# Optimization experiments

Measured on AMD Instinct MI355X. Metric: run time of the kernel, lower is better.

Reference implementation:

```python
import jax, jax.numpy as jnp
import numpy as np

B_, H_, N_, L_ = 4, 512, 64, 2048  # batch, d_model, d_state/2 (conj pairs), seq len


def setup_inputs() -> dict:
    key = jax.random.key(0)
    ks = jax.random.split(key, 8)
    x = jax.random.normal(ks[0], (B_, H_, L_), jnp.float32)
    ln_w = jnp.ones((H_,), jnp.float32)
    ln_b = jnp.zeros((H_,), jnp.float32)
    # S4D-style init: dt log-uniform in [1e-3, 1e-1], A = -1/2 + i*pi*n (S4D-Lin)
    log_dt = jax.random.uniform(ks[1], (H_,), jnp.float32) * (np.log(0.1) - np.log(0.001)) + np.log(0.001)
    log_A_real = jnp.broadcast_to(jnp.log(jnp.float32(0.5)), (H_, N_))
    A_imag = jnp.broadcast_to(np.pi * jnp.arange(N_, dtype=np.float32), (H_, N_))
    B_re = jnp.ones((H_, N_), jnp.float32)
    B_im = jnp.zeros((H_, N_), jnp.float32)
    # 2 kernel channels for bidirectional
    C_re = jax.random.normal(ks[2], (2, H_, N_), jnp.float32) * (0.5 ** 0.5)
    C_im = jax.random.normal(ks[3], (2, H_, N_), jnp.float32) * (0.5 ** 0.5)
    D = jax.random.normal(ks[4], (H_,), jnp.float32)
    W_out = jax.random.normal(ks[5], (H_, H_), jnp.float32) / np.sqrt(H_)
    b_out = jnp.zeros((H_,), jnp.float32)
    return dict(x=x, ln_w=ln_w, ln_b=ln_b, log_dt=log_dt, log_A_real=log_A_real,
                A_imag=A_imag, B_re=B_re, B_im=B_im, C_re=C_re, C_im=C_im,
                D=D, W_out=W_out, b_out=b_out)


def _s4_layer(x, ln_w, ln_b, log_dt, log_A_real, A_imag, B_re, B_im, C_re, C_im, D, W_out, b_out):
    Bb, H, L = x.shape
    # ---- pre-norm LayerNorm over channel dim (module transposes to (B,L,H)) ----
    zt = x.transpose(0, 2, 1)                          # (B, L, H)
    mu = zt.mean(-1, keepdims=True)
    var = jnp.mean((zt - mu) ** 2, -1, keepdims=True)
    zt = (zt - mu) * jax.lax.rsqrt(var + 1e-5) * ln_w + ln_b
    z = zt.transpose(0, 2, 1)                          # (B, H, L)
    # ---- S4 diagonal SSM kernel, ZOH discretization, 2 channels (bidirectional) ----
    dt = jnp.exp(log_dt)[:, None]                      # (H, 1)
    A = -jnp.exp(log_A_real) + 1j * A_imag             # (H, N)
    dtA = A * dt                                       # (H, N)
    dB = (B_re + 1j * B_im) * (jnp.exp(dtA) - 1.0) / A # (H, N) discretized B
    CB = (C_re + 1j * C_im) * dB                       # (2, H, N)
    V = jnp.exp(dtA[:, :, None] * jnp.arange(L))       # (H, N, L) Vandermonde exp(l*dt*A)
    k = 2.0 * jnp.real(jnp.einsum('chn,hnl->chl', CB, V))  # (2, H, L)
    # ---- bidirectional: causal + flipped anticausal kernel, length 2L ----
    zpad = jnp.zeros_like(k[0])
    kb = jnp.concatenate([k[0], zpad], -1) + jnp.concatenate([zpad, k[1][:, ::-1]], -1)  # (H, 2L)
    # ---- FFT convolution ----
    k_f = jnp.fft.rfft(kb, n=2 * L)                    # (H, L+1)
    u_f = jnp.fft.rfft(z, n=2 * L)                     # (B, H, L+1)
    y = jnp.fft.irfft(u_f * k_f, n=2 * L)[..., :L]     # (B, H, L)
    y = y + z * D[:, None]                             # skip connection D*u
    y = jax.nn.gelu(y)                                 # default S4 activation
    y = jnp.einsum('oh,bhl->bol', W_out, y) + b_out[:, None]  # output linear (Conv1d k=1)
    return y + x                                       # residual of S4Layer


def reference(x, ln_w, ln_b, log_dt, log_A_real, A_imag, B_re, B_im, C_re, C_im, D, W_out, b_out):
    return _s4_layer(x, ln_w, ln_b, log_dt, log_A_real, A_imag, B_re, B_im, C_re, C_im, D, W_out, b_out)
```

## Files before the change

kernel.cpp:

```cpp
#include <hip/hip_runtime.h>
#include <math.h>

#define Bq 4
#define Hq 512
#define Nq 64
#define Lq 2048
#define PARAM (Hq*Nq)

__global__ __launch_bounds__(256)
void setup_kernel(const float* __restrict__ log_dt,
                  const float* __restrict__ log_A_real,
                  const float* __restrict__ A_imag,
                  const float* __restrict__ B_re, const float* __restrict__ B_im,
                  const float* __restrict__ C_re, const float* __restrict__ C_im,
                  float* __restrict__ a0, float* __restrict__ b0,
                  float* __restrict__ a1, float* __restrict__ b1,
                  float* __restrict__ pw, float* __restrict__ pwT,
                  const float* __restrict__ x, const float* __restrict__ lnw,
                  const float* __restrict__ lnb, float* __restrict__ z) {
    __shared__ float rs_[16][17], r2_[16][17], mu_s[16], sg_s[16];
    int bx = blockIdx.x;
    if (bx < 128) {
        int idx = bx * 256 + threadIdx.x;
        int h = idx >> 6, n = idx & 63;
        float dt = expf(log_dt[h]);
        float Ar = -expf(log_A_real[idx]);
        float Ai = A_imag[idx];
        float er = expf(Ar * dt);
        float wr = er * cosf(Ai * dt);
        float wi = er * sinf(Ai * dt);
        float mr = wr - 1.0f, mi = wi;
        float den = Ar * Ar + Ai * Ai;
        float qr = (mr * Ar + mi * Ai) / den;
        float qi = (mi * Ar - mr * Ai) / den;
        float Br = B_re[idx], Bi = B_im[idx];
        float dBr = Br * qr - Bi * qi;
        float dBi = Br * qi + Bi * qr;
        float cr = C_re[idx], ci = C_im[idx];
        a0[idx] =  2.0f * (cr * dBr - ci * dBi);
        b0[idx] = -2.0f * (cr * dBi + ci * dBr);
        cr = C_re[PARAM + idx]; ci = C_im[PARAM + idx];
        a1[idx] =  2.0f * (cr * dBr - ci * dBi);
        b1[idx] = -2.0f * (cr * dBi + ci * dBr);
        float c = 1.f, s = 0.f;
        float* base  = pw  + (size_t)h * 65 * 128 + 2 * n;
        float* baseT = pwT + (size_t)(h * 64 + n) * 132;
        for (int d = 0; d <= 64; ++d) {
            *(float2*)(base + (size_t)d * 128) = float2{c, s};
            *(float2*)(baseT + 2 * d)          = float2{c, s};
            float nc = c * wr - s * wi;
            float ns = c * wi + s * wr;
            c = nc; s = ns;
        }
        return;
    }
    int blk = bx - 128;
    int b  = blk / (Lq / 16);
    int l0 = (blk % (Lq / 16)) * 16;
    int tx = threadIdx.x & 15;
    int ty = threadIdx.x >> 4;
    const float* xb = x + (size_t)b * Hq * Lq;
    float s = 0.f, s2 = 0.f;
    for (int h = ty; h < Hq; h += 16) {
        float v = xb[h * Lq + l0 + tx];
        s += v; s2 += v * v;
    }
    rs_[ty][tx] = s; r2_[ty][tx] = s2;
    __syncthreads();
    if (ty == 0) {
        float a = 0.f, c = 0.f;
        #pragma unroll
        for (int i = 0; i < 16; ++i) { a += rs_[i][tx]; c += r2_[i][tx]; }
        float mu = a * (1.0f / Hq);
        float var = c * (1.0f / Hq) - mu * mu;
        mu_s[tx] = mu;
        sg_s[tx] = rsqrtf(var + 1e-5f);
    }
    __syncthreads();
    float mu = mu_s[tx], rs = sg_s[tx];
    float* zb = z + (size_t)b * Hq * Lq;
    for (int h = ty; h < Hq; h += 16) {
        float v = xb[h * Lq + l0 + tx];
        zb[h * Lq + l0 + tx] = (v - mu) * rs * lnw[h] + lnb[h];
    }
}

__global__ __launch_bounds__(256, 4)
void ssm_kernel(const float* __restrict__ z, const float* __restrict__ pw,
                const float* __restrict__ pwT,
                const float* __restrict__ a0, const float* __restrict__ b0,
                const float* __restrict__ a1, const float* __restrict__ b1,
                const float* __restrict__ Dv, float* __restrict__ u) {
    __shared__ float Zs[64][68];
    __shared__ float As[64][68];
    __shared__ float ks0[64], ks1[64], as0_[64], bs0_[64], as1_[64], bs1_[64];
    int h = blockIdx.x, bp = blockIdx.y;
    int t = threadIdx.x;
    int tx = t & 15, ty = t >> 4;
    const float* pwh  = pw  + (size_t)h * 65 * 128;
    const float* pwTh = pwT + (size_t)h * 64 * 132;
    {
        int cc = t & 31, rb = (t >> 5) & 1, jg = t >> 6;
        const float* zb = z + ((size_t)(2 * bp + rb) * Hq + h) * Lq;
        #pragma unroll
        for (int f = 0; f < 4; ++f) {
            float4 v = *(const float4*)(zb + cc * 64 + 16 * jg + 4 * f);
            Zs[16*jg+4*f+0][rb*32+cc] = v.x;
            Zs[16*jg+4*f+1][rb*32+cc] = v.y;
            Zs[16*jg+4*f+2][rb*32+cc] = v.z;
            Zs[16*jg+4*f+3][rb*32+cc] = v.w;
        }
    }
    if (t < 64) {
        as0_[t] = a0[h*64+t]; bs0_[t] = b0[h*64+t];
        as1_[t] = a1[h*64+t]; bs1_[t] = b1[h*64+t];
    }
    __syncthreads();
    if (t < 128) {
        int dir_ = t >> 6, d = t & 63;
        float acc2 = 0.f;
        if (dir_ == 0) {
            for (int n = 0; n < 64; ++n) {
                float2 v = *(const float2*)(pwTh + (size_t)n*132 + 2*d);
                acc2 = fmaf(as0_[n], v.x, acc2);
                acc2 = fmaf(bs0_[n], v.y, acc2);
            }
            ks0[d] = acc2;
        } else {
            for (int n = 0; n < 64; ++n) {
                float2 v = *(const float2*)(pwTh + (size_t)n*132 + 2*d);
                acc2 = fmaf(as1_[n], v.x, acc2);
                acc2 = fmaf(bs1_[n], v.y, acc2);
            }
            ks1[d] = acc2;
        }
    }
    float d0R[4][4] = {}, d0I[4][4] = {}, d1R[4][4] = {}, d1I[4][4] = {};
    #pragma unroll 2
    for (int k = 0; k < 64; ++k) {
        const float4* pr = (const float4*)(pwh + (size_t)k*128 + 8*tx);
        float4 p0 = pr[0], p1 = pr[1];
        float c4[4] = {p0.x, p0.z, p1.x, p1.z};
        float s4[4] = {p0.y, p0.w, p1.y, p1.w};
        float4 zf = *(const float4*)&Zs[63-k][4*ty];
        float4 zg = *(const float4*)&Zs[k][4*ty];
        #pragma unroll
        for (int rr = 0; rr < 4; ++rr) {
            #pragma unroll
            for (int q = 0; q < 4; ++q) {
                float zq0 = (&zf.x)[q], zq1 = (&zg.x)[q];
                d0R[rr][q] = fmaf(c4[rr], zq0, d0R[rr][q]);
                d0I[rr][q] = fmaf(s4[rr], zq0, d0I[rr][q]);
                d1R[rr][q] = fmaf(c4[rr], zq1, d1R[rr][q]);
                d1I[rr][q] = fmaf(s4[rr], zq1, d1I[rr][q]);
            }
        }
    }
    const float4* pr64 = (const float4*)(pwh + (size_t)64*128 + 8*tx);
    float4 w0v = pr64[0], w1v = pr64[1];
    float wc[4] = {w0v.x, w0v.z, w1v.x, w1v.z};
    float wn[4] = {w0v.y, w0v.w, w1v.y, w1v.w};
    int bS = ty >> 3, g = ty & 7;
    float* Vs = &As[0][0];
    #pragma unroll
    for (int rr = 0; rr < 4; ++rr) {
        float vr = 0.f, vi = 0.f;
        #pragma unroll
        for (int q = 0; q < 4; ++q) {
            float nr = fmaf(wc[rr], vr, fmaf(-wn[rr], vi, d0R[rr][q]));
            float ni = fmaf(wn[rr], vr, fmaf(wc[rr], vi, d0I[rr][q]));
            vr = nr; vi = ni;
        }
        *(float2*)(Vs + (size_t)((bS)*8+g)*130 + 2*(4*tx+rr)) = float2{vr, vi};
        vr = 0.f; vi = 0.f;
        #pragma unroll
        for (int q = 3; q >= 0; --q) {
            float nr = fmaf(wc[rr], vr, fmaf(-wn[rr], vi, d1R[rr][q]));
            float ni = fmaf(wn[rr], vr, fmaf(wc[rr], vi, d1I[rr][q]));
            vr = nr; vi = ni;
        }
        *(float2*)(Vs + (size_t)((2+bS)*8+g)*130 + 2*(4*tx+rr)) = float2{vr, vi};
    }
    __syncthreads();
    {
        int dir_ = t >> 7, bS_ = (t >> 6) & 1, n_ = t & 63;
        float2 wv = *(const float2*)(pwh + (size_t)64*128 + 2*n_);
        float w2r = fmaf(wv.x, wv.x, -(wv.y*wv.y));
        float w2i = 2.f*wv.x*wv.y;
        float Tr = fmaf(w2r, w2r, -(w2i*w2i));
        float Ti = 2.f*w2r*w2i;
        float* row = Vs + (size_t)(dir_*2+bS_)*8*130 + 2*n_;
        float er = 0.f, ei = 0.f;
        #pragma unroll
        for (int s2 = 0; s2 < 8; ++s2) {
            int g2 = dir_ ? (7 - s2) : s2;
            float* p2 = row + g2*130;
            float vr2 = p2[0], vi2 = p2[1];
            p2[0] = er; p2[1] = ei;
            float nr = fmaf(Tr, er, fmaf(-Ti, ei, vr2));
            float ni = fmaf(Ti, er, fmaf(Tr, ei, vi2));
            er = nr; ei = ni;
        }
    }
    __syncthreads();
    #pragma unroll
    for (int rr = 0; rr < 4; ++rr) {
        float2 E0 = *(const float2*)(Vs + (size_t)((bS)*8+g)*130 + 2*(4*tx+rr));
        float trr = E0.x, tii = E0.y;
        #pragma unroll
        for (int q = 0; q < 4; ++q) {
            float dr = d0R[rr][q], di = d0I[rr][q];
            d0R[rr][q] = trr; d0I[rr][q] = tii;
            float nr = fmaf(wc[rr], trr, fmaf(-wn[rr], tii, dr));
            float ni = fmaf(wn[rr], trr, fmaf(wc[rr], tii, di));
            trr = nr; tii = ni;
        }
        float2 E1 = *(const float2*)(Vs + (size_t)((2+bS)*8+g)*130 + 2*(4*tx+rr));
        trr = E1.x; tii = E1.y;
        #pragma unroll
        for (int q = 3; q >= 0; --q) {
            float dr = d1R[rr][q], di = d1I[rr][q];
            d1R[rr][q] = trr; d1I[rr][q] = tii;
            float nr = fmaf(wc[rr], trr, fmaf(-wn[rr], tii, dr));
            float ni = fmaf(wn[rr], trr, fmaf(wc[rr], tii, di));
            trr = nr; tii = ni;
        }
    }
    __syncthreads();
    int si = t & 63, kg = t >> 6;
    float2 pv[8];
    float acc[4][4] = {};
    for (int p = 0; p < 5; ++p) {
        if (p == 0) {
            #pragma unroll
            for (int q = 0; q < 16; ++q) {
                int kk = 16*kg + q;
                int d = si - kk;
                As[kk][si] = (d >= 0) ? ks0[d] : ks1[-d-1];
            }
        } else {
            const float* as_ = (p < 3) ? as0_ : as1_;
            const float* bs_ = (p < 3) ? bs0_ : bs1_;
            #pragma unroll
            for (int q = 0; q < 16; ++q) {
                int j = q >> 1;
                int n = 32*((p < 3) ? (p-1) : (p-3)) + 8*kg + j;
                float vx = pv[j].x, vy = pv[j].y;
                As[16*kg+q][si] = ((q&1) == 0) ? fmaf(as_[n], vx, bs_[n]*vy)
                                               : fmaf(bs_[n], vx, -as_[n]*vy);
            }
            if (p == 1 && tx < 8) {
                #pragma unroll
                for (int rr = 0; rr < 4; ++rr) {
                    int ml = 8*tx + 2*rr;
                    float4 vR; vR.x = d0R[rr][0]; vR.y = d0R[rr][1];
                    vR.z = d0R[rr][2]; vR.w = d0R[rr][3];
                    float4 vI; vI.x = d0I[rr][0]; vI.y = d0I[rr][1];
                    vI.z = d0I[rr][2]; vI.w = d0I[rr][3];
                    *(float4*)&Zs[ml][4*ty]   = vR;
                    *(float4*)&Zs[ml+1][4*ty] = vI;
                }
            } else if (p == 2 && tx >= 8) {
                #pragma unroll
                for (int rr = 0; rr < 4; ++rr) {
                    int ml = 8*(tx-8) + 2*rr;
                    float4 vR; vR.x = d0R[rr][0]; vR.y = d0R[rr][1];
                    vR.z = d0R[rr][2]; vR.w = d0R[rr][3];
                    float4 vI; vI.x = d0I[rr][0]; vI.y = d0I[rr][1];
                    vI.z = d0I[rr][2]; vI.w = d0I[rr][3];
                    *(float4*)&Zs[ml][4*ty]   = vR;
                    *(float4*)&Zs[ml+1][4*ty] = vI;
                }
            } else if (p == 3 && tx < 8) {
                #pragma unroll
                for (int rr = 0; rr < 4; ++rr) {
                    int ml = 8*tx + 2*rr;
                    float4 vR; vR.x = d1R[rr][0]; vR.y = d1R[rr][1];
                    vR.z = d1R[rr][2]; vR.w = d1R[rr][3];
                    float4 vI; vI.x = d1I[rr][0]; vI.y = d1I[rr][1];
                    vI.z = d1I[rr][2]; vI.w = d1I[rr][3];
                    *(float4*)&Zs[ml][4*ty]   = vR;
                    *(float4*)&Zs[ml+1][4*ty] = vI;
                }
            } else if (p == 4 && tx >= 8) {
                #pragma unroll
                for (int rr = 0; rr < 4; ++rr) {
                    int ml = 8*(tx-8) + 2*rr;
                    float4 vR; vR.x = d1R[rr][0]; vR.y = d1R[rr][1];
                    vR.z = d1R[rr][2]; vR.w = d1R[rr][3];
                    float4 vI; vI.x = d1I[rr][0]; vI.y = d1I[rr][1];
                    vI.z = d1I[rr][2]; vI.w = d1I[rr][3];
                    *(float4*)&Zs[ml][4*ty]   = vR;
                    *(float4*)&Zs[ml+1][4*ty] = vI;
                }
            }
        }
        __syncthreads();
        if (p < 4) {
            int pn = p + 1;
            int pp = (pn < 3) ? (pn-1) : (pn-3);
            int dsel = (pn < 3) ? (si + 1) : (63 - si);
            #pragma unroll
            for (int j2 = 0; j2 < 8; ++j2) {
                int n = 32*pp + 8*kg + j2;
                pv[j2] = *(const float2*)(pwTh + (size_t)n*132 + 2*dsel);
            }
        }
        #pragma unroll 8
        for (int kk = 0; kk < 64; ++kk) {
            float4 av = *(const float4*)&As[kk][4*tx];
            float4 bv = *(const float4*)&Zs[kk][4*ty];
            #pragma unroll
            for (int ii = 0; ii < 4; ++ii) {
                float a = (&av.x)[ii];
                acc[ii][0] = fmaf(a, bv.x, acc[ii][0]);
                acc[ii][1] = fmaf(a, bv.y, acc[ii][1]);
                acc[ii][2] = fmaf(a, bv.z, acc[ii][2]);
                acc[ii][3] = fmaf(a, bv.w, acc[ii][3]);
            }
        }
        __syncthreads();
    }
    float dv = Dv[h];
    #pragma unroll
    for (int q = 0; q < 4; ++q) {
        int cc2 = 4*ty + q;
        int b2 = 2*bp + (cc2 >> 5), ch2 = cc2 & 31;
        size_t base = ((size_t)b2 * Hq + h) * Lq + ch2 * 64 + 4 * tx;
        float4 zr = *(const float4*)(z + base);
        float vv[4];
        vv[0] = acc[0][q] + dv * zr.x;
        vv[1] = acc[1][q] + dv * zr.y;
        vv[2] = acc[2][q] + dv * zr.z;
        vv[3] = acc[3][q] + dv * zr.w;
        #pragma unroll
        for (int i = 0; i < 4; ++i) {
            float v = vv[i];
            float tt = tanhf(0.7978845608028654f * (v + 0.044715f * v * v * v));
            vv[i] = 0.5f * v * (1.0f + tt);
        }
        float4 r; r.x = vv[0]; r.y = vv[1]; r.z = vv[2]; r.w = vv[3];
        *(float4*)(u + base) = r;
    }
}

__global__ __launch_bounds__(512, 4)
void gemm_kernel(const float* __restrict__ u, const float* __restrict__ W,
                 const float* __restrict__ bias, const float* __restrict__ x,
                 float* __restrict__ out) {
    int l0 = blockIdx.x * 64;
    int o0 = blockIdx.y * 128;
    int b  = blockIdx.z;
    int tid = threadIdx.x;
    __shared__ float Ws[2][32][132];
    __shared__ float Us[2][32][68];
    const float* ub = u + (size_t)b * Hq * Lq;
    float acc[4][4] = {};
    int wo = tid >> 4, wl = tid & 15;
    int sj = tid & 31, so = tid >> 5;
    int sl = tid & 63, sk = tid >> 6;
    float wreg[8], ureg[4];
    #pragma unroll
    for (int r = 0; r < 8; ++r) wreg[r] = W[(size_t)(o0 + so + 16*r) * Hq + sj];
    #pragma unroll
    for (int r = 0; r < 4; ++r) ureg[r] = ub[(size_t)(4*sk + r) * Lq + l0 + sl];
    #pragma unroll
    for (int r = 0; r < 8; ++r) Ws[0][sj][so + 16*r] = wreg[r];
    #pragma unroll
    for (int r = 0; r < 4; ++r) Us[0][4*sk + r][sl] = ureg[r];
    __syncthreads();
    for (int t = 0; t < Hq / 32; ++t) {
        int cur = t & 1;
        if (t < 15) {
            int k0 = (t + 1) * 32;
            #pragma unroll
            for (int r = 0; r < 8; ++r)
                wreg[r] = W[(size_t)(o0 + so + 16*r) * Hq + k0 + sj];
            #pragma unroll
            for (int r = 0; r < 4; ++r)
                ureg[r] = ub[(size_t)(k0 + 4*sk + r) * Lq + l0 + sl];
        }
        #pragma unroll 8
        for (int j = 0; j < 32; ++j) {
            float4 av = *(const float4*)&Ws[cur][j][4 * wo];
            float4 bv = *(const float4*)&Us[cur][j][4 * wl];
            #pragma unroll
            for (int io = 0; io < 4; ++io) {
                float a = (&av.x)[io];
                acc[io][0] = fmaf(a, bv.x, acc[io][0]);
                acc[io][1] = fmaf(a, bv.y, acc[io][1]);
                acc[io][2] = fmaf(a, bv.z, acc[io][2]);
                acc[io][3] = fmaf(a, bv.w, acc[io][3]);
            }
        }
        if (t < 15) {
            int nxt = cur ^ 1;
            #pragma unroll
            for (int r = 0; r < 8; ++r) Ws[nxt][sj][so + 16*r] = wreg[r];
            #pragma unroll
            for (int r = 0; r < 4; ++r) Us[nxt][4*sk + r][sl] = ureg[r];
        }
        __syncthreads();
    }
    #pragma unroll
    for (int io = 0; io < 4; ++io) {
        int o = o0 + 4 * wo + io;
        float bo = bias[o];
        size_t base = ((size_t)b * Hq + o) * Lq + l0 + 4 * wl;
        const float4 xr = *(const float4*)(x + base);
        float4 r;
        r.x = acc[io][0] + bo + xr.x;
        r.y = acc[io][1] + bo + xr.y;
        r.z = acc[io][2] + bo + xr.z;
        r.w = acc[io][3] + bo + xr.w;
        *(float4*)(out + base) = r;
    }
}

extern "C" void kernel_launch(void* const* d_in, const int* in_sizes, int n_in,
                              void* d_out, int out_size, void* d_ws, size_t ws_size,
                              hipStream_t stream) {
    (void)in_sizes; (void)n_in; (void)out_size; (void)ws_size;
    const float* x          = (const float*)d_in[0];
    const float* ln_w       = (const float*)d_in[1];
    const float* ln_b       = (const float*)d_in[2];
    const float* log_dt     = (const float*)d_in[3];
    const float* log_A_real = (const float*)d_in[4];
    const float* A_imag     = (const float*)d_in[5];
    const float* B_re       = (const float*)d_in[6];
    const float* B_im       = (const float*)d_in[7];
    const float* C_re       = (const float*)d_in[8];
    const float* C_im       = (const float*)d_in[9];
    const float* Dv         = (const float*)d_in[10];
    const float* W          = (const float*)d_in[11];
    const float* b_out      = (const float*)d_in[12];
    float* out = (float*)d_out;
    float* ws  = (float*)d_ws;

    const size_t BHL = (size_t)Bq * Hq * Lq;
    float* a0  = ws;
    float* b0  = ws + (size_t)PARAM;
    float* a1  = ws + 2 * (size_t)PARAM;
    float* b1  = ws + 3 * (size_t)PARAM;
    float* pw  = ws + 4 * (size_t)PARAM;
    float* pwT = ws + 134 * (size_t)PARAM;
    float* z   = ws + 266 * (size_t)PARAM;
    float* u   = z + BHL;

    setup_kernel<<<128 + Bq * (Lq / 16), 256, 0, stream>>>(
        log_dt, log_A_real, A_imag, B_re, B_im, C_re, C_im,
        a0, b0, a1, b1, pw, pwT, x, ln_w, ln_b, z);
    ssm_kernel<<<dim3(Hq, 2), 256, 0, stream>>>(z, pw, pwT, a0, b0, a1, b1,
                                                Dv, u);
    gemm_kernel<<<dim3(Lq / 64, Hq / 128, Bq), 512, 0, stream>>>(u, W, b_out, x, out);
}
```

Baseline: 276.3 us.

## Swizzle Zs shared-memory columns, batch power-table stores, relax occupancy bound

Applies an XOR swizzle to the Zs shared tile's column index on every read and write, aiming to reduce LDS bank conflicts, especially on the transposing scalar stores at load time. The setup kernel now computes the power table in chunks of 16 in registers before writing both layouts, so the stores are grouped. Launch bounds for the SSM kernel drop the minimum-blocks hint from 4 to 3, giving the compiler more registers per thread at the risk of lower occupancy. There is also a risk that a read or write of Zs in the unseen parts of the kernel still uses unswizzled indices.

New measurement: 274.4 us. About the same (-0.7%).

```diff
diff --git a/kernel.cpp b/kernel.cpp
--- a/kernel.cpp
+++ b/kernel.cpp
@@ -6,6 +6,8 @@
 #define Nq 64
 #define Lq 2048
 #define PARAM (Hq*Nq)
+
+#define ZSW(row, col) ((col) ^ ((((row) >> 3) & 7) << 2))
 
 __global__ __launch_bounds__(256)
 void setup_kernel(const float* __restrict__ log_dt,
@@ -43,15 +45,27 @@
         a1[idx] =  2.0f * (cr * dBr - ci * dBi);
         b1[idx] = -2.0f * (cr * dBi + ci * dBr);
         float c = 1.f, s = 0.f;
-        float* base  = pw  + (size_t)h * 65 * 128 + 2 * n;
-        float* baseT = pwT + (size_t)(h * 64 + n) * 132;
-        for (int d = 0; d <= 64; ++d) {
-            *(float2*)(base + (size_t)d * 128) = float2{c, s};
-            *(float2*)(baseT + 2 * d)          = float2{c, s};
-            float nc = c * wr - s * wi;
-            float ns = c * wi + s * wr;
-            c = nc; s = ns;
-        }
+        float* basep = pw  + (size_t)h * 65 * 128 + 2 * n;
+        float* baset = pwT + (size_t)(h * 64 + n) * 132;
+        #pragma unroll
+        for (int ch = 0; ch < 4; ++ch) {
+            float2 pr[16];
+            #pragma unroll
+            for (int dd = 0; dd < 16; ++dd) {
+                pr[dd] = float2{c, s};
+                float nc = c * wr - s * wi;
+                float ns = c * wi + s * wr;
+                c = nc; s = ns;
+            }
+            #pragma unroll
+            for (int dd = 0; dd < 16; ++dd)
+                *(float2*)(basep + (size_t)(ch * 16 + dd) * 128) = pr[dd];
+            #pragma unroll
+            for (int dd = 0; dd < 16; ++dd)
+                *(float2*)(baset + 2 * (ch * 16 + dd)) = pr[dd];
+        }
+        *(float2*)(basep + (size_t)64 * 128) = float2{c, s};
+        *(float2*)(baset + 128)              = float2{c, s};
         return;
     }
     int blk = bx - 128;
@@ -85,7 +99,7 @@
     }
 }
 
-__global__ __launch_bounds__(256, 4)
+__global__ __launch_bounds__(256, 3)
 void ssm_kernel(const float* __restrict__ z, const float* __restrict__ pw,
                 const float* __restrict__ pwT,
                 const float* __restrict__ a0, const float* __restrict__ b0,
@@ -102,13 +116,15 @@
     {
         int cc = t & 31, rb = (t >> 5) & 1, jg = t >> 6;
         const float* zb = z + ((size_t)(2 * bp + rb) * Hq + h) * Lq;
+        int c0 = rb * 32 + cc;
         #pragma unroll
         for (int f = 0; f < 4; ++f) {
             float4 v = *(const float4*)(zb + cc * 64 + 16 * jg + 4 * f);
-            Zs[16*jg+4*f+0][rb*32+cc] = v.x;
-            Zs[16*jg+4*f+1][rb*32+cc] = v.y;
-            Zs[16*jg+4*f+2][rb*32+cc] = v.z;
-            Zs[16*jg+4*f+3][rb*32+cc] = v.w;
+            int r0 = 16*jg + 4*f;
+            Zs[r0+0][ZSW(r0+0, c0)] = v.x;
+            Zs[r0+1][ZSW(r0+1, c0)] = v.y;
+            Zs[r0+2][ZSW(r0+2, c0)] = v.z;
+            Zs[r0+3][ZSW(r0+3, c0)] = v.w;
         }
     }
     if (t < 64) {
@@ -142,8 +158,9 @@
         float4 p0 = pr[0], p1 = pr[1];
         float c4[4] = {p0.x, p0.z, p1.x, p1.z};
         float s4[4] = {p0.y, p0.w, p1.y, p1.w};
-        float4 zf = *(const float4*)&Zs[63-k][4*ty];
-        float4 zg = *(const float4*)&Zs[k][4*ty];
+        int rf = 63 - k;
+        float4 zf = *(const float4*)&Zs[rf][ZSW(rf, 4*ty)];
+        float4 zg = *(const float4*)&Zs[k][ZSW(k, 4*ty)];
         #pragma unroll
         for (int rr = 0; rr < 4; ++rr) {
             #pragma unroll
@@ -257,8 +274,8 @@
                     vR.z = d0R[rr][2]; vR.w = d0R[rr][3];
                     float4 vI; vI.x = d0I[rr][0]; vI.y = d0I[rr][1];
                     vI.z = d0I[rr][2]; vI.w = d0I[rr][3];
-                    *(float4*)&Zs[ml][4*ty]   = vR;
-                    *(float4*)&Zs[ml+1][4*ty] = vI;
+                    *(float4*)&Zs[ml][ZSW(ml, 4*ty)]     = vR;
+                    *(float4*)&Zs[ml+1][ZSW(ml+1, 4*ty)] = vI;
                 }
             } else if (p == 2 && tx >= 8) {
                 #pragma unroll
@@ -268,8 +285,8 @@
                     vR.z = d0R[rr][2]; vR.w = d0R[rr][3];
                     float4 vI; vI.x = d0I[rr][0]; vI.y = d0I[rr][1];
                     vI.z = d0I[rr][2]; vI.w = d0I[rr][3];
-                    *(float4*)&Zs[ml][4*ty]   = vR;
-                    *(float4*)&Zs[ml+1][4*ty] = vI;
+                    *(float4*)&Zs[ml][ZSW(ml, 4*ty)]     = vR;
+                    *(float4*)&Zs[ml+1][ZSW(ml+1, 4*ty)] = vI;
                 }
             } else if (p == 3 && tx < 8) {
                 #pragma unroll
@@ -279,8 +296,8 @@
                     vR.z = d1R[rr][2]; vR.w = d1R[rr][3];
                     float4 vI; vI.x = d1I[rr][0]; vI.y = d1I[rr][1];
                     vI.z = d1I[rr][2]; vI.w = d1I[rr][3];
-                    *(float4*)&Zs[ml][4*ty]   = vR;
-                    *(float4*)&Zs[ml+1][4*ty] = vI;
+                    *(float4*)&Zs[ml][ZSW(ml, 4*ty)]     = vR;
+                    *(float4*)&Zs[ml+1][ZSW(ml+1, 4*ty)] = vI;
                 }
             } else if (p == 4 && tx >= 8) {
                 #pragma unroll
@@ -290,8 +307,8 @@
                     vR.z = d1R[rr][2]; vR.w = d1R[rr][3];
                     float4 vI; vI.x = d1I[rr][0]; vI.y = d1I[rr][1];
                     vI.z = d1I[rr][2]; vI.w = d1I[rr][3];
-                    *(float4*)&Zs[ml][4*ty]   = vR;
-                    *(float4*)&Zs[ml+1][4*ty] = vI;
+                    *(float4*)&Zs[ml][ZSW(ml, 4*ty)]     = vR;
+                    *(float4*)&Zs[ml+1][ZSW(ml+1, 4*ty)] = vI;
                 }
             }
         }
@@ -309,7 +326,7 @@
         #pragma unroll 8
         for (int kk = 0; kk < 64; ++kk) {
             float4 av = *(const float4*)&As[kk][4*tx];
-            float4 bv = *(const float4*)&Zs[kk][4*ty];
+            float4 bv = *(const float4*)&Zs[kk][ZSW(kk, 4*ty)];
             #pragma unroll
             for (int ii = 0; ii < 4; ++ii) {
                 float a = (&av.x)[ii];
```
